# Kernel tuning notes

Measured on AMD Instinct MI355X. Metric: run time of the kernel, lower is better.

The kernel has to match this reference:

```python
import jax, jax.numpy as jnp
import numpy as np

B, CQ, CKV, H, W = 16, 512, 512, 48, 48
NH = 8
HD = CQ // NH
SCALE = HD ** -0.5


def setup_inputs() -> dict:
    key = jax.random.key(0)
    ks = jax.random.split(key, 11)
    s = 0.02
    return {
        "query_features": jax.random.normal(ks[0], (B, CQ, H, W), jnp.float32),
        "key_features": jax.random.normal(ks[1], (B, CKV, H, W), jnp.float32),
        "value_features": jax.random.normal(ks[2], (B, CKV, H, W), jnp.float32),
        "Wq": jax.random.normal(ks[3], (CQ, CQ), jnp.float32) * s,
        "bq": jnp.zeros((CQ,), jnp.float32),
        "Wk": jax.random.normal(ks[4], (CQ, CKV), jnp.float32) * s,
        "bk": jnp.zeros((CQ,), jnp.float32),
        "Wv": jax.random.normal(ks[5], (CQ, CKV), jnp.float32) * s,
        "bv": jnp.zeros((CQ,), jnp.float32),
        "Wo": jax.random.normal(ks[6], (CQ, CQ), jnp.float32) * s,
        "bo": jnp.zeros((CQ,), jnp.float32),
    }


def _proj(x, Wt, b):
    # 1x1 conv == channel GEMM: (O,C) x (B,C,H,W) -> (B,O,H,W)
    return jnp.einsum('oc,bchw->bohw', Wt, x) + b[None, :, None, None]


def reference(query_features, key_features, value_features,
              Wq, bq, Wk, bk, Wv, bv, Wo, bo):
    b, cq, h, w = query_features.shape
    hw = h * w
    Q = _proj(query_features, Wq, bq).reshape(b, NH, HD, hw)
    K = _proj(key_features, Wk, bk).reshape(b, NH, HD, hw)
    V = _proj(value_features, Wv, bv).reshape(b, NH, HD, hw)
    # NOTE: faithful to source — contraction is over the SPATIAL axis d=H*W,
    # so scores are (B, NH, HD, HD) (head_dim x head_dim attention).
    scores = jnp.einsum('bnhd,bnkd->bnhk', Q, K) * SCALE
    attn = jax.nn.softmax(scores, axis=-1)
    out = jnp.einsum('bnhk,bnkd->bnhd', attn, V)  # (B, NH, HD, HW)
    out = out.reshape(b, cq, h, w)
    return _proj(out, Wo, bo)
```

## Files before the change

### kernel.cpp

```cpp
#include <hip/hip_runtime.h>
#include <hip/hip_bf16.h>

#define B_   16
#define C_   512
#define HW_  2304
#define NH_  8
#define HD_  64
#define SCALE_ 0.125f

typedef __bf16 bf16x8 __attribute__((ext_vector_type(8)));
typedef __bf16 bf16x4 __attribute__((ext_vector_type(4)));
typedef float  f32x4  __attribute__((ext_vector_type(4)));

#define MFMA16(a, b, c) __builtin_amdgcn_mfma_f32_16x16x32_bf16((a), (b), (c), 0, 0, 0)

__device__ __forceinline__ void gload_lds16(const void* g, void* l) {
    __builtin_amdgcn_global_load_lds(
        (const __attribute__((address_space(1))) unsigned int*)g,
        (__attribute__((address_space(3))) unsigned int*)l, 16, 0, 0);
}

__global__ __launch_bounds__(256) void transpose_cvt(
    const float* __restrict__ X, __bf16* __restrict__ XT)
{
    const int b  = blockIdx.z;
    const int c0 = blockIdx.y * 64;
    const int h0 = blockIdx.x * 128;
    const float* Xb = X + (size_t)b * C_ * HW_;
    __bf16* XTb = XT + (size_t)b * HW_ * C_;

    __shared__ float Ts[64 * 129];
    const int t = threadIdx.x;

    #pragma unroll
    for (int p = 0; p < 8; ++p) {
        const int c  = p * 8 + (t >> 5);
        const int hg = (t & 31) * 4;
        const float4 v = *(const float4*)&Xb[(size_t)(c0 + c) * HW_ + h0 + hg];
        Ts[c * 129 + hg + 0] = v.x;
        Ts[c * 129 + hg + 1] = v.y;
        Ts[c * 129 + hg + 2] = v.z;
        Ts[c * 129 + hg + 3] = v.w;
    }
    __syncthreads();
    #pragma unroll
    for (int p = 0; p < 4; ++p) {
        const int hw = p * 32 + (t >> 3);
        const int g  = (t & 7) * 8;
        bf16x8 o;
        #pragma unroll
        for (int e = 0; e < 8; ++e)
            o[e] = (__bf16)Ts[(g + e) * 129 + hw];
        *(bf16x8*)&XTb[(size_t)(h0 + hw) * C_ + c0 + g] = o;
    }
}

__global__ __launch_bounds__(256) void proj_gemm(
    const __bf16* __restrict__ XT, const float* __restrict__ W,
    const float* __restrict__ bias, __bf16* __restrict__ Y)
{
    const int b  = blockIdx.z;
    const int n0 = blockIdx.x * 128;
    const int m0 = blockIdx.y * 128;
    const __bf16* XTb = XT + (size_t)b * HW_ * C_;
    __bf16* Yb = Y + (size_t)b * C_ * HW_;

    __shared__ __align__(16) __bf16 As[128 * 64];
    __shared__ __align__(16) __bf16 Bs[128 * 64];

    const int t = threadIdx.x;
    const int w = t >> 6, lane = t & 63, l16 = lane & 15, q = lane >> 4;
    const int wm = w >> 1, wn = w & 1;

    const int ar = t >> 4;
    const int ak = (t & 15) * 4;
    const int br = lane >> 3;
    const int bg = (lane & 7) * 8;

    f32x4 acc[4][4] = {};

    for (int ks = 0; ks < 8; ++ks) {
        const int k0 = ks * 64;
        __syncthreads();
        #pragma unroll
        for (int pb = 0; pb < 4; ++pb) {
            const int rbase = pb * 32 + w * 8;
            gload_lds16(&XTb[(size_t)(n0 + rbase + br) * C_ + k0 + bg],
                        &Bs[rbase * 64]);
        }
        #pragma unroll
        for (int pa = 0; pa < 8; ++pa) {
            const int row = pa * 16 + ar;
            const float4 f = *(const float4*)&W[(size_t)(m0 + row) * C_ + k0 + ak];
            bf16x4 v;
            v[0] = (__bf16)f.x; v[1] = (__bf16)f.y;
            v[2] = (__bf16)f.z; v[3] = (__bf16)f.w;
            *(bf16x4*)&As[row * 64 + ak] = v;
        }
        __syncthreads();
        #pragma unroll
        for (int kk = 0; kk < 2; ++kk) {
            bf16x8 af[4], bfr[4];
            #pragma unroll
            for (int mi = 0; mi < 4; ++mi)
                af[mi] = *(bf16x8*)&As[(wm * 64 + mi * 16 + l16) * 64 + kk * 32 + q * 8];
            #pragma unroll
            for (int ni = 0; ni < 4; ++ni)
                bfr[ni] = *(bf16x8*)&Bs[(wn * 64 + ni * 16 + l16) * 64 + kk * 32 + q * 8];
            #pragma unroll
            for (int mi = 0; mi < 4; ++mi)
                #pragma unroll
                for (int ni = 0; ni < 4; ++ni)
                    acc[mi][ni] = MFMA16(af[mi], bfr[ni], acc[mi][ni]);
        }
    }

    #pragma unroll
    for (int mi = 0; mi < 4; ++mi) {
        #pragma unroll
        for (int r = 0; r < 4; ++r) {
            const int m = m0 + wm * 64 + mi * 16 + q * 4 + r;
            const float bv_ = bias[m];
            #pragma unroll
            for (int ni = 0; ni < 4; ++ni) {
                const int n = n0 + wn * 64 + ni * 16 + l16;
                Yb[(size_t)m * HW_ + n] = (__bf16)(acc[mi][ni][r] + bv_);
            }
        }
    }
}

__global__ __launch_bounds__(256) void attn_scores_part(
    const __bf16* __restrict__ Qw, const __bf16* __restrict__ Kw,
    float* __restrict__ Sp)
{
    const int bn  = blockIdx.x;
    const int kcs = blockIdx.y;
    const __bf16* Qb = Qw + (size_t)bn * 64 * HW_;
    const __bf16* Kb = Kw + (size_t)bn * 64 * HW_;

    __shared__ __align__(16) __bf16 Qs[64 * 72];
    __shared__ __align__(16) __bf16 Ks[64 * 72];

    const int t    = threadIdx.x;
    const int w    = t >> 6;
    const int lane = t & 63;
    const int l16  = lane & 15;
    const int q    = lane >> 4;
    const int row  = t >> 2;
    const int kc   = (t & 3) * 16;

    f32x4 acc[4] = {};

    for (int it = 0; it < 6; ++it) {
        const int k0 = kcs * 384 + it * 64;
        __syncthreads();
        *(bf16x8*)&Qs[row * 72 + kc]     = *(const bf16x8*)&Qb[(size_t)row * HW_ + k0 + kc];
        *(bf16x8*)&Qs[row * 72 + kc + 8] = *(const bf16x8*)&Qb[(size_t)row * HW_ + k0 + kc + 8];
        *(bf16x8*)&Ks[row * 72 + kc]     = *(const bf16x8*)&Kb[(size_t)row * HW_ + k0 + kc];
        *(bf16x8*)&Ks[row * 72 + kc + 8] = *(const bf16x8*)&Kb[(size_t)row * HW_ + k0 + kc + 8];
        __syncthreads();
        #pragma unroll
        for (int kk = 0; kk < 2; ++kk) {
            const bf16x8 a = *(bf16x8*)&Qs[(w * 16 + l16) * 72 + kk * 32 + q * 8];
            #pragma unroll
            for (int ni = 0; ni < 4; ++ni) {
                const bf16x8 bb = *(bf16x8*)&Ks[(ni * 16 + l16) * 72 + kk * 32 + q * 8];
                acc[ni] = MFMA16(a, bb, acc[ni]);
            }
        }
    }

    float* S = Sp + ((size_t)kcs * 128 + bn) * 4096;
    #pragma unroll
    for (int r = 0; r < 4; ++r)
        #pragma unroll
        for (int ni = 0; ni < 4; ++ni)
            S[(w * 16 + q * 4 + r) * 64 + ni * 16 + l16] = acc[ni][r];
}

__global__ __launch_bounds__(256) void softmax_reduce(
    const float* __restrict__ Sp, __bf16* __restrict__ Pw)
{
    const int bn = blockIdx.x;
    const int t  = threadIdx.x;
    const int r  = t >> 2;
    const int c0 = (t & 3) * 16;

    float v[16];
    #pragma unroll
    for (int j = 0; j < 16; ++j) v[j] = 0.f;
    #pragma unroll
    for (int kc = 0; kc < 6; ++kc) {
        const float* s = Sp + ((size_t)kc * 128 + bn) * 4096 + r * 64 + c0;
        #pragma unroll
        for (int j4 = 0; j4 < 4; ++j4) {
            const float4 f = *(const float4*)&s[j4 * 4];
            v[j4 * 4 + 0] += f.x; v[j4 * 4 + 1] += f.y;
            v[j4 * 4 + 2] += f.z; v[j4 * 4 + 3] += f.w;
        }
    }
    float mx = -1e30f;
    #pragma unroll
    for (int j = 0; j < 16; ++j) { v[j] *= SCALE_; mx = fmaxf(mx, v[j]); }
    mx = fmaxf(mx, __shfl_xor(mx, 1));
    mx = fmaxf(mx, __shfl_xor(mx, 2));
    float s = 0.f;
    #pragma unroll
    for (int j = 0; j < 16; ++j) { v[j] = __expf(v[j] - mx); s += v[j]; }
    s += __shfl_xor(s, 1);
    s += __shfl_xor(s, 2);
    const float inv = 1.f / s;
    bf16x8 o0, o1;
    #pragma unroll
    for (int j = 0; j < 8; ++j) {
        o0[j] = (__bf16)(v[j] * inv);
        o1[j] = (__bf16)(v[8 + j] * inv);
    }
    *(bf16x8*)&Pw[(size_t)bn * 4096 + r * 64 + c0]     = o0;
    *(bf16x8*)&Pw[(size_t)bn * 4096 + r * 64 + c0 + 8] = o1;
}

__global__ __launch_bounds__(256) void attn_pv(
    const __bf16* __restrict__ Pw, const __bf16* __restrict__ Vw,
    __bf16* __restrict__ AOT)
{
    const int dsl = blockIdx.x;
    const int bn  = blockIdx.y;
    const int t    = threadIdx.x;
    const int w    = t >> 6;
    const int lane = t & 63;
    const int l16  = lane & 15;
    const int q    = lane >> 4;

    __shared__ __align__(16) __bf16 Ps[64 * 72];
    __shared__ __align__(16) __bf16 Vt[4][16 * 264];

    {
        const int row = t >> 2;
        const int kc  = (t & 3) * 16;
        *(bf16x8*)&Ps[row * 72 + kc]     = *(const bf16x8*)&Pw[(size_t)bn * 4096 + row * 64 + kc];
        *(bf16x8*)&Ps[row * 72 + kc + 8] = *(const bf16x8*)&Pw[(size_t)bn * 4096 + row * 64 + kc + 8];
    }

    const __bf16* Vb = Vw + (size_t)bn * 64 * HW_;
    const int d0w = dsl * 256 + w * 64;
    {
        const int m4 = lane & 15;
        const int kh = (lane >> 4) * 16;
        __bf16 rr[4][16];
        #pragma unroll
        for (int j = 0; j < 16; ++j) {
            const bf16x4 v = *(const bf16x4*)&Vb[(size_t)(kh + j) * HW_ + d0w + 4 * m4];
            #pragma unroll
            for (int e = 0; e < 4; ++e) rr[e][j] = v[e];
        }
        #pragma unroll
        for (int e = 0; e < 4; ++e) {
            bf16x8 s0, s1;
            #pragma unroll
            for (int j = 0; j < 8; ++j) { s0[j] = rr[e][j]; s1[j] = rr[e][8 + j]; }
            *(bf16x8*)&Vt[w][m4 * 264 + e * 64 + kh]     = s0;
            *(bf16x8*)&Vt[w][m4 * 264 + e * 64 + kh + 8] = s1;
        }
    }
    __syncthreads();

    f32x4 acc[4][4] = {};
    #pragma unroll
    for (int kk = 0; kk < 2; ++kk) {
        bf16x8 af[4], bfr[4];
        #pragma unroll
        for (int mi = 0; mi < 4; ++mi)
            af[mi] = *(bf16x8*)&Ps[(mi * 16 + l16) * 72 + kk * 32 + q * 8];
        #pragma unroll
        for (int ni = 0; ni < 4; ++ni) {
            const int dl = ni * 16 + l16;
            bfr[ni] = *(bf16x8*)&Vt[w][(dl >> 2) * 264 + (dl & 3) * 64 + kk * 32 + q * 8];
        }
        #pragma unroll
        for (int mi = 0; mi < 4; ++mi)
            #pragma unroll
            for (int ni = 0; ni < 4; ++ni)
                acc[mi][ni] = MFMA16(af[mi], bfr[ni], acc[mi][ni]);
    }

    const int bb = bn >> 3;
    const int nh = bn & 7;
    #pragma unroll
    for (int mi = 0; mi < 4; ++mi)
        #pragma unroll
        for (int ni = 0; ni < 4; ++ni) {
            const int d = d0w + ni * 16 + l16;
            bf16x4 o;
            #pragma unroll
            for (int r = 0; r < 4; ++r) o[r] = (__bf16)acc[mi][ni][r];
            *(bf16x4*)&AOT[((size_t)bb * HW_ + d) * C_ + nh * 64 + mi * 16 + q * 4] = o;
        }
}

__global__ __launch_bounds__(256) void proj_out(
    const __bf16* __restrict__ AOT, const float* __restrict__ W,
    const float* __restrict__ bias, float* __restrict__ out)
{
    const int b  = blockIdx.z;
    const int n0 = blockIdx.x * 128;
    const int m0 = blockIdx.y * 128;
    const __bf16* XTb = AOT + (size_t)b * HW_ * C_;
    float* Yb = out + (size_t)b * C_ * HW_;

    __shared__ __align__(16) __bf16 As[128 * 64];
    __shared__ __align__(16) __bf16 Bs[128 * 64];

    const int t = threadIdx.x;
    const int w = t >> 6, lane = t & 63, l16 = lane & 15, q = lane >> 4;
    const int wm = w >> 1, wn = w & 1;

    const int ar = t >> 4;
    const int ak = (t & 15) * 4;
    const int br = lane >> 3;
    const int bg = (lane & 7) * 8;

    f32x4 acc[4][4] = {};

    for (int ks = 0; ks < 8; ++ks) {
        const int k0 = ks * 64;
        __syncthreads();
        #pragma unroll
        for (int pb = 0; pb < 4; ++pb) {
            const int rbase = pb * 32 + w * 8;
            gload_lds16(&XTb[(size_t)(n0 + rbase + br) * C_ + k0 + bg],
                        &Bs[rbase * 64]);
        }
        #pragma unroll
        for (int pa = 0; pa < 8; ++pa) {
            const int row = pa * 16 + ar;
            const float4 f = *(const float4*)&W[(size_t)(m0 + row) * C_ + k0 + ak];
            bf16x4 v;
            v[0] = (__bf16)f.x; v[1] = (__bf16)f.y;
            v[2] = (__bf16)f.z; v[3] = (__bf16)f.w;
            *(bf16x4*)&As[row * 64 + ak] = v;
        }
        __syncthreads();
        #pragma unroll
        for (int kk = 0; kk < 2; ++kk) {
            bf16x8 af[4], bfr[4];
            #pragma unroll
            for (int mi = 0; mi < 4; ++mi)
                af[mi] = *(bf16x8*)&As[(wm * 64 + mi * 16 + l16) * 64 + kk * 32 + q * 8];
            #pragma unroll
            for (int ni = 0; ni < 4; ++ni)
                bfr[ni] = *(bf16x8*)&Bs[(wn * 64 + ni * 16 + l16) * 64 + kk * 32 + q * 8];
            #pragma unroll
            for (int mi = 0; mi < 4; ++mi)
                #pragma unroll
                for (int ni = 0; ni < 4; ++ni)
                    acc[mi][ni] = MFMA16(af[mi], bfr[ni], acc[mi][ni]);
        }
    }

    #pragma unroll
    for (int mi = 0; mi < 4; ++mi) {
        #pragma unroll
        for (int r = 0; r < 4; ++r) {
            const int m = m0 + wm * 64 + mi * 16 + q * 4 + r;
            const float bv_ = bias[m];
            #pragma unroll
            for (int ni = 0; ni < 4; ++ni) {
                const int n = n0 + wn * 64 + ni * 16 + l16;
                Yb[(size_t)m * HW_ + n] = acc[mi][ni][r] + bv_;
            }
        }
    }
}

extern "C" void kernel_launch(void* const* d_in, const int* in_sizes, int n_in,
                              void* d_out, int out_size, void* d_ws, size_t ws_size,
                              hipStream_t stream)
{
    (void)in_sizes; (void)n_in; (void)out_size; (void)ws_size;
    const float* qf = (const float*)d_in[0];
    const float* kf = (const float*)d_in[1];
    const float* vf = (const float*)d_in[2];
    const float* Wq = (const float*)d_in[3];
    const float* bq = (const float*)d_in[4];
    const float* Wk = (const float*)d_in[5];
    const float* bk = (const float*)d_in[6];
    const float* Wv = (const float*)d_in[7];
    const float* bv = (const float*)d_in[8];
    const float* Wo = (const float*)d_in[9];
    const float* bo = (const float*)d_in[10];

    const size_t QE = (size_t)B_ * C_ * HW_;
    __bf16* region0 = (__bf16*)d_ws;
    __bf16* XT  = region0;
    float*  Sp  = (float*)region0;
    __bf16* AOT = region0;
    __bf16* Qw  = region0 + QE;
    __bf16* Kw  = Qw + QE;
    __bf16* Vw  = Kw + QE;
    __bf16* Pw  = Vw + QE;

    transpose_cvt<<<dim3(18, 8, 16), 256, 0, stream>>>(qf, XT);
    proj_gemm    <<<dim3(18, 4, 16), 256, 0, stream>>>(XT, Wq, bq, Qw);
    transpose_cvt<<<dim3(18, 8, 16), 256, 0, stream>>>(kf, XT);
    proj_gemm    <<<dim3(18, 4, 16), 256, 0, stream>>>(XT, Wk, bk, Kw);
    transpose_cvt<<<dim3(18, 8, 16), 256, 0, stream>>>(vf, XT);
    proj_gemm    <<<dim3(18, 4, 16), 256, 0, stream>>>(XT, Wv, bv, Vw);

    attn_scores_part<<<dim3(128, 6), 256, 0, stream>>>(Qw, Kw, Sp);
    softmax_reduce  <<<dim3(128),    256, 0, stream>>>(Sp, Pw);
    attn_pv         <<<dim3(9, 128), 256, 0, stream>>>(Pw, Vw, AOT);
    proj_out        <<<dim3(18, 4, 16), 256, 0, stream>>>(AOT, Wo, bo, (float*)d_out);
}
```

Measured before the change: 488.4 us.

## Pre-convert weights to bf16 and stream GEMM tiles via swizzled direct-to-LDS loads

Weights are converted to bf16 once, by an extra z-slice of the transpose kernel and by extra blocks in attn_pv for Wo. The projection GEMMs can then load both operands with global_load_lds into XOR-swizzled shared memory, instead of doing per-tile fp32 loads, conversion and LDS stores. The scores kernel also switches to swizzled direct-to-LDS loads and fewer K-splits (4 instead of 6), which reduces partial-score traffic in the softmax reduce. The risk is workspace aliasing: Wb shares its slot with Pw and WoB sits in Qw, and the swizzle indexing has to be correct.

After: 424.8 us. -13.0%, faster.

```diff
diff --git a/kernel.cpp b/kernel.cpp
--- a/kernel.cpp
+++ b/kernel.cpp
@@ -20,9 +20,24 @@
         (__attribute__((address_space(3))) unsigned int*)l, 16, 0, 0);
 }
 
-__global__ __launch_bounds__(256) void transpose_cvt(
-    const float* __restrict__ X, __bf16* __restrict__ XT)
-{
+__global__ __launch_bounds__(256) void prep(
+    const float* __restrict__ X, __bf16* __restrict__ XT,
+    const float* __restrict__ W, __bf16* __restrict__ Wb)
+{
+    const int t = threadIdx.x;
+    if (blockIdx.z == 16) {
+        const int bid = blockIdx.y * 18 + blockIdx.x;
+        if (bid < 128) {
+            const int idx = bid * 2048 + t * 8;
+            const float4 f0 = *(const float4*)&W[idx];
+            const float4 f1 = *(const float4*)&W[idx + 4];
+            bf16x8 o;
+            o[0] = (__bf16)f0.x; o[1] = (__bf16)f0.y; o[2] = (__bf16)f0.z; o[3] = (__bf16)f0.w;
+            o[4] = (__bf16)f1.x; o[5] = (__bf16)f1.y; o[6] = (__bf16)f1.z; o[7] = (__bf16)f1.w;
+            *(bf16x8*)&Wb[idx] = o;
+        }
+        return;
+    }
     const int b  = blockIdx.z;
     const int c0 = blockIdx.y * 64;
     const int h0 = blockIdx.x * 128;
@@ -30,7 +45,6 @@
     __bf16* XTb = XT + (size_t)b * HW_ * C_;
 
     __shared__ float Ts[64 * 129];
-    const int t = threadIdx.x;
 
     #pragma unroll
     for (int p = 0; p < 8; ++p) {
@@ -55,27 +69,20 @@
     }
 }
 
-__global__ __launch_bounds__(256) void proj_gemm(
-    const __bf16* __restrict__ XT, const float* __restrict__ W,
-    const float* __restrict__ bias, __bf16* __restrict__ Y)
-{
-    const int b  = blockIdx.z;
-    const int n0 = blockIdx.x * 128;
-    const int m0 = blockIdx.y * 128;
-    const __bf16* XTb = XT + (size_t)b * HW_ * C_;
-    __bf16* Yb = Y + (size_t)b * C_ * HW_;
-
+template <typename OUT_T>
+__device__ __forceinline__ void gemm_body(
+    const __bf16* __restrict__ XTb, const __bf16* __restrict__ Wb,
+    const float* __restrict__ bias, OUT_T* __restrict__ Yb,
+    int n0, int m0)
+{
     __shared__ __align__(16) __bf16 As[128 * 64];
     __shared__ __align__(16) __bf16 Bs[128 * 64];
 
     const int t = threadIdx.x;
     const int w = t >> 6, lane = t & 63, l16 = lane & 15, q = lane >> 4;
     const int wm = w >> 1, wn = w & 1;
-
-    const int ar = t >> 4;
-    const int ak = (t & 15) * 4;
-    const int br = lane >> 3;
-    const int bg = (lane & 7) * 8;
+    const int sr = lane >> 3;
+    const int sg = ((lane & 7) ^ (lane >> 3)) * 8;
 
     f32x4 acc[4][4] = {};
 
@@ -83,30 +90,22 @@
         const int k0 = ks * 64;
         __syncthreads();
         #pragma unroll
-        for (int pb = 0; pb < 4; ++pb) {
-            const int rbase = pb * 32 + w * 8;
-            gload_lds16(&XTb[(size_t)(n0 + rbase + br) * C_ + k0 + bg],
-                        &Bs[rbase * 64]);
-        }
-        #pragma unroll
-        for (int pa = 0; pa < 8; ++pa) {
-            const int row = pa * 16 + ar;
-            const float4 f = *(const float4*)&W[(size_t)(m0 + row) * C_ + k0 + ak];
-            bf16x4 v;
-            v[0] = (__bf16)f.x; v[1] = (__bf16)f.y;
-            v[2] = (__bf16)f.z; v[3] = (__bf16)f.w;
-            *(bf16x4*)&As[row * 64 + ak] = v;
+        for (int p = 0; p < 4; ++p) {
+            const int rb = p * 32 + w * 8;
+            gload_lds16(&Wb [(size_t)(m0 + rb + sr) * C_ + k0 + sg], &As[rb * 64]);
+            gload_lds16(&XTb[(size_t)(n0 + rb + sr) * C_ + k0 + sg], &Bs[rb * 64]);
         }
         __syncthreads();
         #pragma unroll
         for (int kk = 0; kk < 2; ++kk) {
+            const int sw = ((kk * 4 + q) ^ (l16 & 7)) * 8;
             bf16x8 af[4], bfr[4];
             #pragma unroll
             for (int mi = 0; mi < 4; ++mi)
-                af[mi] = *(bf16x8*)&As[(wm * 64 + mi * 16 + l16) * 64 + kk * 32 + q * 8];
+                af[mi] = *(bf16x8*)&As[(wm * 64 + mi * 16 + l16) * 64 + sw];
             #pragma unroll
             for (int ni = 0; ni < 4; ++ni)
-                bfr[ni] = *(bf16x8*)&Bs[(wn * 64 + ni * 16 + l16) * 64 + kk * 32 + q * 8];
+                bfr[ni] = *(bf16x8*)&Bs[(wn * 64 + ni * 16 + l16) * 64 + sw];
             #pragma unroll
             for (int mi = 0; mi < 4; ++mi)
                 #pragma unroll
@@ -124,10 +123,28 @@
             #pragma unroll
             for (int ni = 0; ni < 4; ++ni) {
                 const int n = n0 + wn * 64 + ni * 16 + l16;
-                Yb[(size_t)m * HW_ + n] = (__bf16)(acc[mi][ni][r] + bv_);
+                Yb[(size_t)m * HW_ + n] = (OUT_T)(acc[mi][ni][r] + bv_);
             }
         }
     }
+}
+
+__global__ __launch_bounds__(256) void proj_gemm(
+    const __bf16* __restrict__ XT, const __bf16* __restrict__ Wb,
+    const float* __restrict__ bias, __bf16* __restrict__ Y)
+{
+    const int b = blockIdx.z;
+    gemm_body<__bf16>(XT + (size_t)b * HW_ * C_, Wb, bias,
+                      Y + (size_t)b * C_ * HW_, blockIdx.x * 128, blockIdx.y * 128);
+}
+
+__global__ __launch_bounds__(256) void proj_out(
+    const __bf16* __restrict__ AOT, const __bf16* __restrict__ Wb,
+    const float* __restrict__ bias, float* __restrict__ out)
+{
+    const int b = blockIdx.z;
+    gemm_body<float>(AOT + (size_t)b * HW_ * C_, Wb, bias,
+                     out + (size_t)b * C_ * HW_, blockIdx.x * 128, blockIdx.y * 128);
 }
 
 __global__ __launch_bounds__(256) void attn_scores_part(
@@ -139,33 +156,36 @@
     const __bf16* Qb = Qw + (size_t)bn * 64 * HW_;
     const __bf16* Kb = Kw + (size_t)bn * 64 * HW_;
 
-    __shared__ __align__(16) __bf16 Qs[64 * 72];
-    __shared__ __align__(16) __bf16 Ks[64 * 72];
+    __shared__ __align__(16) __bf16 Qs[64 * 64];
+    __shared__ __align__(16) __bf16 Ks[64 * 64];
 
     const int t    = threadIdx.x;
     const int w    = t >> 6;
     const int lane = t & 63;
     const int l16  = lane & 15;
     const int q    = lane >> 4;
-    const int row  = t >> 2;
-    const int kc   = (t & 3) * 16;
+    const int sr   = lane >> 3;
+    const int sg   = ((lane & 7) ^ (lane >> 3)) * 8;
 
     f32x4 acc[4] = {};
 
-    for (int it = 0; it < 6; ++it) {
-        const int k0 = kcs * 384 + it * 64;
+    for (int it = 0; it < 9; ++it) {
+        const int k0 = kcs * 576 + it * 64;
         __syncthreads();
-        *(bf16x8*)&Qs[row * 72 + kc]     = *(const bf16x8*)&Qb[(size_t)row * HW_ + k0 + kc];
-        *(bf16x8*)&Qs[row * 72 + kc + 8] = *(const bf16x8*)&Qb[(size_t)row * HW_ + k0 + kc + 8];
-        *(bf16x8*)&Ks[row * 72 + kc]     = *(const bf16x8*)&Kb[(size_t)row * HW_ + k0 + kc];
-        *(bf16x8*)&Ks[row * 72 + kc + 8] = *(const bf16x8*)&Kb[(size_t)row * HW_ + k0 + kc + 8];
+        #pragma unroll
+        for (int p = 0; p < 2; ++p) {
+            const int rb = w * 16 + p * 8;
+            gload_lds16(&Qb[(size_t)(rb + sr) * HW_ + k0 + sg], &Qs[rb * 64]);
+            gload_lds16(&Kb[(size_t)(rb + sr) * HW_ + k0 + sg], &Ks[rb * 64]);
+        }
         __syncthreads();
         #pragma unroll
         for (int kk = 0; kk < 2; ++kk) {
-            const bf16x8 a = *(bf16x8*)&Qs[(w * 16 + l16) * 72 + kk * 32 + q * 8];
+            const int sw = ((kk * 4 + q) ^ (l16 & 7)) * 8;
+            const bf16x8 a = *(bf16x8*)&Qs[(w * 16 + l16) * 64 + sw];
             #pragma unroll
             for (int ni = 0; ni < 4; ++ni) {
-                const bf16x8 bb = *(bf16x8*)&Ks[(ni * 16 + l16) * 72 + kk * 32 + q * 8];
+                const bf16x8 bb = *(bf16x8*)&Ks[(ni * 16 + l16) * 64 + sw];
                 acc[ni] = MFMA16(a, bb, acc[ni]);
             }
         }
@@ -191,7 +211,7 @@
     #pragma unroll
     for (int j = 0; j < 16; ++j) v[j] = 0.f;
     #pragma unroll
-    for (int kc = 0; kc < 6; ++kc) {
+    for (int kc = 0; kc < 4; ++kc) {
         const float* s = Sp + ((size_t)kc * 128 + bn) * 4096 + r * 64 + c0;
         #pragma unroll
         for (int j4 = 0; j4 < 4; ++j4) {
@@ -223,11 +243,21 @@
 
 __global__ __launch_bounds__(256) void attn_pv(
     const __bf16* __restrict__ Pw, const __bf16* __restrict__ Vw,
-    __bf16* __restrict__ AOT)
-{
+    __bf16* __restrict__ AOT, const float* __restrict__ Wo, __bf16* __restrict__ WoB)
+{
+    const int t = threadIdx.x;
+    if (blockIdx.x == 9) {
+        const int idx = blockIdx.y * 2048 + t * 8;
+        const float4 f0 = *(const float4*)&Wo[idx];
+        const float4 f1 = *(const float4*)&Wo[idx + 4];
+        bf16x8 o;
+        o[0] = (__bf16)f0.x; o[1] = (__bf16)f0.y; o[2] = (__bf16)f0.z; o[3] = (__bf16)f0.w;
+        o[4] = (__bf16)f1.x; o[5] = (__bf16)f1.y; o[6] = (__bf16)f1.z; o[7] = (__bf16)f1.w;
+        *(bf16x8*)&WoB[idx] = o;
+        return;
+    }
     const int dsl = blockIdx.x;
     const int bn  = blockIdx.y;
-    const int t    = threadIdx.x;
     const int w    = t >> 6;
     const int lane = t & 63;
     const int l16  = lane & 15;
@@ -297,81 +327,6 @@
             for (int r = 0; r < 4; ++r) o[r] = (__bf16)acc[mi][ni][r];
             *(bf16x4*)&AOT[((size_t)bb * HW_ + d) * C_ + nh * 64 + mi * 16 + q * 4] = o;
         }
-}
-
-__global__ __launch_bounds__(256) void proj_out(
-    const __bf16* __restrict__ AOT, const float* __restrict__ W,
-    const float* __restrict__ bias, float* __restrict__ out)
-{
-    const int b  = blockIdx.z;
-    const int n0 = blockIdx.x * 128;
-    const int m0 = blockIdx.y * 128;
-    const __bf16* XTb = AOT + (size_t)b * HW_ * C_;
-    float* Yb = out + (size_t)b * C_ * HW_;
-
-    __shared__ __align__(16) __bf16 As[128 * 64];
-    __shared__ __align__(16) __bf16 Bs[128 * 64];
-
-    const int t = threadIdx.x;
-    const int w = t >> 6, lane = t & 63, l16 = lane & 15, q = lane >> 4;
-    const int wm = w >> 1, wn = w & 1;
-
-    const int ar = t >> 4;
-    const int ak = (t & 15) * 4;
-    const int br = lane >> 3;
-    const int bg = (lane & 7) * 8;
-
-    f32x4 acc[4][4] = {};
-
-    for (int ks = 0; ks < 8; ++ks) {
-        const int k0 = ks * 64;
-        __syncthreads();
-        #pragma unroll
-        for (int pb = 0; pb < 4; ++pb) {
-            const int rbase = pb * 32 + w * 8;
-            gload_lds16(&XTb[(size_t)(n0 + rbase + br) * C_ + k0 + bg],
-                        &Bs[rbase * 64]);
-        }
-        #pragma unroll
-        for (int pa = 0; pa < 8; ++pa) {
-            const int row = pa * 16 + ar;
-            const float4 f = *(const float4*)&W[(size_t)(m0 + row) * C_ + k0 + ak];
-            bf16x4 v;
-            v[0] = (__bf16)f.x; v[1] = (__bf16)f.y;
-            v[2] = (__bf16)f.z; v[3] = (__bf16)f.w;
-            *(bf16x4*)&As[row * 64 + ak] = v;
-        }
-        __syncthreads();
-        #pragma unroll
-        for (int kk = 0; kk < 2; ++kk) {
-            bf16x8 af[4], bfr[4];
-            #pragma unroll
-            for (int mi = 0; mi < 4; ++mi)
-                af[mi] = *(bf16x8*)&As[(wm * 64 + mi * 16 + l16) * 64 + kk * 32 + q * 8];
-            #pragma unroll
-            for (int ni = 0; ni < 4; ++ni)
-                bfr[ni] = *(bf16x8*)&Bs[(wn * 64 + ni * 16 + l16) * 64 + kk * 32 + q * 8];
-            #pragma unroll
-            for (int mi = 0; mi < 4; ++mi)
-                #pragma unroll
-                for (int ni = 0; ni < 4; ++ni)
-                    acc[mi][ni] = MFMA16(af[mi], bfr[ni], acc[mi][ni]);
-        }
-    }
-
-    #pragma unroll
-    for (int mi = 0; mi < 4; ++mi) {
-        #pragma unroll
-        for (int r = 0; r < 4; ++r) {
-            const int m = m0 + wm * 64 + mi * 16 + q * 4 + r;
-            const float bv_ = bias[m];
-            #pragma unroll
-            for (int ni = 0; ni < 4; ++ni) {
-                const int n = n0 + wn * 64 + ni * 16 + l16;
-                Yb[(size_t)m * HW_ + n] = acc[mi][ni][r] + bv_;
-            }
-        }
-    }
 }
 
 extern "C" void kernel_launch(void* const* d_in, const int* in_sizes, int n_in,
@@ -399,17 +354,20 @@
     __bf16* Qw  = region0 + QE;
     __bf16* Kw  = Qw + QE;
     __bf16* Vw  = Kw + QE;
-    __bf16* Pw  = Vw + QE;
-
-    transpose_cvt<<<dim3(18, 8, 16), 256, 0, stream>>>(qf, XT);
-    proj_gemm    <<<dim3(18, 4, 16), 256, 0, stream>>>(XT, Wq, bq, Qw);
-    transpose_cvt<<<dim3(18, 8, 16), 256, 0, stream>>>(kf, XT);
-    proj_gemm    <<<dim3(18, 4, 16), 256, 0, stream>>>(XT, Wk, bk, Kw);
-    transpose_cvt<<<dim3(18, 8, 16), 256, 0, stream>>>(vf, XT);
-    proj_gemm    <<<dim3(18, 4, 16), 256, 0, stream>>>(XT, Wv, bv, Vw);
-
-    attn_scores_part<<<dim3(128, 6), 256, 0, stream>>>(Qw, Kw, Sp);
+    __bf16* slotP = Vw + QE;
+    __bf16* Wb  = slotP;
+    __bf16* Pw  = slotP;
+    __bf16* WoB = Qw;
+
+    prep     <<<dim3(18, 8, 17), 256, 0, stream>>>(qf, XT, Wq, Wb);
+    proj_gemm<<<dim3(18, 4, 16), 256, 0, stream>>>(XT, Wb, bq, Qw);
+    prep     <<<dim3(18, 8, 17), 256, 0, stream>>>(kf, XT, Wk, Wb);
+    proj_gemm<<<dim3(18, 4, 16), 256, 0, stream>>>(XT, Wb, bk, Kw);
+    prep     <<<dim3(18, 8, 17), 256, 0, stream>>>(vf, XT, Wv, Wb);
+    proj_gemm<<<dim3(18, 4, 16), 256, 0, stream>>>(XT, Wb, bv, Vw);
+
+    attn_scores_part<<<dim3(128, 4), 256, 0, stream>>>(Qw, Kw, Sp);
     softmax_reduce  <<<dim3(128),    256, 0, stream>>>(Sp, Pw);
-    attn_pv         <<<dim3(9, 128), 256, 0, stream>>>(Pw, Vw, AOT);
-    proj_out        <<<dim3(18, 4, 16), 256, 0, stream>>>(AOT, Wo, bo, (float*)d_out);
-}
+    attn_pv         <<<dim3(10, 128), 256, 0, stream>>>(Pw, Vw, AOT, Wo, WoB);
+    proj_out        <<<dim3(18, 4, 16), 256, 0, stream>>>(AOT, WoB, bo, (float*)d_out);
+}
```
